# Kernel tuning notes

Measured on AMD Instinct MI355X. Metric: run time of the kernel, lower is better.

Reference implementation:

```python
import jax, jax.numpy as jnp
import numpy as np

N_NODES = 50000
N_EDGES = 600000
N_FEAT = 256
N_HID = 128
N_CLASS = 64
HEADS = 8
LEAKY_SLOPE = 0.2


def setup_inputs() -> dict:
    key = jax.random.key(0)
    ks = jax.random.split(key, 12)
    D0 = N_HID // HEADS  # 16 per-head dim, layer 0
    x = jax.random.normal(ks[0], (N_NODES, N_FEAT), dtype=jnp.float32)
    edge_index = jax.random.randint(ks[1], (2, N_EDGES), 0, N_NODES, dtype=jnp.int64)
    s0 = 1.0 / np.sqrt(N_FEAT)
    s1 = 1.0 / np.sqrt(N_HID)
    return {
        "x": x,
        "edge_index": edge_index,
        "W0": jax.random.normal(ks[2], (N_FEAT, HEADS * D0), dtype=jnp.float32) * s0,
        "a_src0": jax.random.normal(ks[3], (HEADS, D0), dtype=jnp.float32) * s0,
        "a_dst0": jax.random.normal(ks[4], (HEADS, D0), dtype=jnp.float32) * s0,
        "b0": jnp.zeros((HEADS * D0,), dtype=jnp.float32),
        "W1": jax.random.normal(ks[5], (N_HID, HEADS * N_CLASS), dtype=jnp.float32) * s1,
        "a_src1": jax.random.normal(ks[6], (HEADS, N_CLASS), dtype=jnp.float32) * s1,
        "a_dst1": jax.random.normal(ks[7], (HEADS, N_CLASS), dtype=jnp.float32) * s1,
        "b1": jnp.zeros((N_CLASS,), dtype=jnp.float32),
    }


def gat_conv(x, src, dst, W, a_s, a_d, b, concat, num_nodes):
    H, D = a_s.shape
    h = (x @ W).reshape(-1, H, D)                    # [N, H, D]
    alpha_s = jnp.einsum('nhd,hd->nh', h, a_s)       # [N, H]
    alpha_d = jnp.einsum('nhd,hd->nh', h, a_d)       # [N, H]
    e = jax.nn.leaky_relu(alpha_s[src] + alpha_d[dst], LEAKY_SLOPE)  # [E, H]
    # numerically stable edge-softmax grouped by destination node
    m = jax.ops.segment_max(e, dst, num_segments=num_nodes)
    m = jnp.where(jnp.isfinite(m), m, 0.0)           # nodes with no in-edges
    ex = jnp.exp(e - m[dst])
    denom = jax.ops.segment_sum(ex, dst, num_segments=num_nodes)
    alpha = ex / (denom[dst] + 1e-16)                # [E, H]
    msg = h[src] * alpha[:, :, None]                 # [E, H, D]
    out = jax.ops.segment_sum(msg, dst, num_segments=num_nodes)  # [N, H, D]
    if concat:
        out = out.reshape(num_nodes, H * D)
    else:
        out = out.mean(axis=1)
    return out + b


def reference(x, edge_index, W0, a_src0, a_dst0, b0, W1, a_src1, a_dst1, b1):
    src, dst = edge_index[0], edge_index[1]
    h = gat_conv(x, src, dst, W0, a_src0, a_dst0, b0, True, N_NODES)
    h = jax.nn.elu(h)  # eval mode: dropout is identity
    h = gat_conv(h, src, dst, W1, a_src1, a_dst1, b1, False, N_NODES)
    return jax.nn.log_softmax(h, axis=-1)
```

## Files before the change

kernel.cpp:

```cpp
#include <hip/hip_runtime.h>
#include <hip/hip_bf16.h>
#include <math.h>

#define NN 50000
#define NE 600000
#define NF 256
#define NHID 128
#define HEADS 8
#define D0 16
#define NCLS 64
#define NB1 196

#define PK0 (9 * 8 * 64 * 8)
#define PK1 (4 * 32 * 64 * 8)
#define PKA (4 * 64 * 8)
#define CASTN (NN * NF / 4)
#define PREPN (PK0 + PK1 + PKA)

typedef __attribute__((ext_vector_type(8))) short short8;
typedef __attribute__((ext_vector_type(4))) float floatx4;

__device__ __forceinline__ float bf16lo(uint v) { return __uint_as_float((v & 0xffffu) << 16); }
__device__ __forceinline__ float bf16hi(uint v) { return __uint_as_float(v & 0xffff0000u); }
__device__ __forceinline__ uint packbf16(float a, float b) {
    return (uint)__bfloat16_as_ushort(__float2bfloat16(a)) |
           ((uint)__bfloat16_as_ushort(__float2bfloat16(b)) << 16);
}
__device__ __forceinline__ short f2bf(float v) {
    return (short)__bfloat16_as_ushort(__float2bfloat16(v));
}
__device__ __forceinline__ float bf16tof(short v) {
    return __uint_as_float(((uint)(ushort)v) << 16);
}


__global__ void scan1_kernel(const int* __restrict__ deg, int* __restrict__ rs,
                             int* __restrict__ bsum) {
    __shared__ int sh[256];
    int tid = threadIdx.x;
    int i = blockIdx.x * 256 + tid;
    int v = (i < NN) ? deg[i] : 0;
    sh[tid] = v;
    __syncthreads();
    for (int off = 1; off < 256; off <<= 1) {
        int t = (tid >= off) ? sh[tid - off] : 0;
        __syncthreads();
        sh[tid] += t;
        __syncthreads();
    }
    if (i < NN) rs[i] = sh[tid] - v;
    if (tid == 255) bsum[blockIdx.x] = sh[255];
}

__global__ void scan2_kernel(const int* __restrict__ bsum, int* __restrict__ bsumx) {
    __shared__ int sh[256];
    int tid = threadIdx.x;
    int v = (tid < NB1) ? bsum[tid] : 0;
    sh[tid] = v;
    __syncthreads();
    for (int off = 1; off < 256; off <<= 1) {
        int t = (tid >= off) ? sh[tid - off] : 0;
        __syncthreads();
        sh[tid] += t;
        __syncthreads();
    }
    if (tid < NB1) bsumx[tid] = sh[tid] - v;
}

__global__ void scan3_kernel(int* __restrict__ rs, const int* __restrict__ bsumx) {
    int i = blockIdx.x * 256 + threadIdx.x;
    if (i < NN) rs[i] += bsumx[i >> 8];
}

__global__ void scatter_kernel(const int* __restrict__ ei, const int* __restrict__ rs,
                               int* __restrict__ cnt2, int* __restrict__ csr) {
    int e = blockIdx.x * 256 + threadIdx.x;
    if (e >= NE) return;
    int s = ei[e], d = ei[NE + e];
    int pos = rs[d] + atomicAdd(&cnt2[d], 1);
    csr[pos] = s;
}


__global__ void fused_prep_kernel(const float* __restrict__ x, short* __restrict__ xb,
                                  const int* __restrict__ ei, int* __restrict__ deg,
                                  const float* __restrict__ W0, const float* __restrict__ aS0,
                                  const float* __restrict__ aD0, const float* __restrict__ W1,
                                  const float* __restrict__ aS1, const float* __restrict__ aD1,
                                  short* __restrict__ Bp0, short* __restrict__ Bp1,
                                  short* __restrict__ wA1b) {
    int i = blockIdx.x * 256 + threadIdx.x;
    if (i < CASTN) {
        float4 v = ((const float4*)x)[i];
        short4 r;
        r.x = f2bf(v.x); r.y = f2bf(v.y); r.z = f2bf(v.z); r.w = f2bf(v.w);
        ((short4*)xb)[i] = r;
        return;
    }
    int e = i - CASTN;
    if (e < NE) {
        atomicAdd(&deg[ei[NE + e]], 1);
        return;
    }
    int tid = e - NE;
    if (tid < PK0) {
        int j = tid & 7, l = (tid >> 3) & 63, ks = (tid >> 9) & 7, t = tid >> 12;
        int k = ks * 32 + (l >> 4) * 8 + j;
        float v;
        if (t < 8) {
            int c = t * 16 + (l & 15);
            v = W0[(size_t)k * 128 + c];
        } else {
            int jj = l & 15;
            int hh = jj & 7;
            const float* av = (jj < 8) ? aS0 : aD0;
            float sum = 0.f;
            for (int dd = 0; dd < D0; ++dd)
                sum += W0[(size_t)k * 128 + hh * D0 + dd] * av[hh * D0 + dd];
            v = sum;
        }
        Bp0[tid] = f2bf(v);
    } else if (tid < PK0 + PK1) {
        int t2 = tid - PK0;
        int j = t2 & 7, l = (t2 >> 3) & 63, ks = (t2 >> 9) & 31, t = t2 >> 14;
        int kk = ks * 32 + (l >> 4) * 8 + j;
        int c = t * 16 + (l & 15);
        Bp1[t2] = f2bf(W1[(size_t)(kk & 127) * 512 + (kk >> 7) * 64 + c] * 0.125f);
    } else if (tid < PREPN) {
        int t3 = tid - PK0 - PK1;
        int j = t3 & 7, l = (t3 >> 3) & 63, ks = t3 >> 9;
        int k = ks * 32 + (l >> 4) * 8 + j;
        int c = l & 15;
        int h = c & 7;
        const float* av = (c < 8) ? aS1 : aD1;
        float sum = 0.f;
        for (int d2 = 0; d2 < NCLS; ++d2)
            sum += W1[(size_t)k * 512 + h * NCLS + d2] * av[h * NCLS + d2];
        wA1b[t3] = f2bf(sum);
    }
}


__global__ __launch_bounds__(256) void gemm0_mfma(const short* __restrict__ xb,
                                                  const short* __restrict__ Bp,
                                                  ushort* __restrict__ h0b,
                                                  float* __restrict__ as0,
                                                  float* __restrict__ ad0) {
    int lane = threadIdx.x & 63, wave = threadIdx.x >> 6;
    int rg = wave >> 1, cg = wave & 1;
    int q = lane >> 4, c16 = lane & 15;
    int row0 = blockIdx.x * 32 + rg * 16;
    int arow = row0 + c16;
    if (arow > NN - 1) arow = NN - 1;
    const short* ap = xb + (size_t)arow * NF + q * 8;
    floatx4 acc[5] = {};
#pragma unroll
    for (int ks = 0; ks < 8; ++ks) {
        short8 af = *(const short8*)(ap + ks * 32);
#pragma unroll
        for (int tt = 0; tt < 4; ++tt) {
            int t = cg * 4 + tt;
            short8 bf = *(const short8*)(Bp + (((size_t)t * 8 + ks) * 64 + lane) * 8);
            acc[tt] = __builtin_amdgcn_mfma_f32_16x16x32_bf16(af, bf, acc[tt], 0, 0, 0);
        }
        if (cg) {
            short8 bf = *(const short8*)(Bp + (((size_t)8 * 8 + ks) * 64 + lane) * 8);
            acc[4] = __builtin_amdgcn_mfma_f32_16x16x32_bf16(af, bf, acc[4], 0, 0, 0);
        }
    }
#pragma unroll
    for (int r = 0; r < 4; ++r) {
        int grow = row0 + q * 4 + r;
        if (grow >= NN) continue;
#pragma unroll
        for (int tt = 0; tt < 4; ++tt)
            h0b[(size_t)grow * NHID + cg * 64 + tt * 16 + c16] =
                (ushort)f2bf(acc[tt][r]);
        if (cg) {
            float v = acc[4][r];
            if (c16 < 8) as0[grow * 8 + c16] = v;
            else         ad0[grow * 8 + (c16 - 8)] = v;
        }
    }
}

__global__ __launch_bounds__(256) void alpha1_mfma(const ushort* __restrict__ x1b,
                                                   const short* __restrict__ wA1b,
                                                   float* __restrict__ as1,
                                                   float* __restrict__ ad1) {
    int lane = threadIdx.x & 63, wave = threadIdx.x >> 6;
    int q = lane >> 4, c16 = lane & 15;
    int row0 = blockIdx.x * 64 + wave * 16;
    int arow = row0 + c16;
    if (arow > NN - 1) arow = NN - 1;
    const short* ap = (const short*)x1b + (size_t)arow * NHID + q * 8;
    floatx4 acc = {};
#pragma unroll
    for (int ks = 0; ks < 4; ++ks) {
        short8 af = *(const short8*)(ap + ks * 32);
        short8 bf = *(const short8*)(wA1b + (((size_t)ks) * 64 + lane) * 8);
        acc = __builtin_amdgcn_mfma_f32_16x16x32_bf16(af, bf, acc, 0, 0, 0);
    }
#pragma unroll
    for (int r = 0; r < 4; ++r) {
        int grow = row0 + q * 4 + r;
        if (grow >= NN) continue;
        float v = acc[r];
        if (c16 < 8) as1[grow * 8 + c16] = v;
        else         ad1[grow * 8 + (c16 - 8)] = v;
    }
}

__global__ __launch_bounds__(256) void gemm1_mfma(const short* __restrict__ AGG,
                                                  const short* __restrict__ Bp,
                                                  const float* __restrict__ b1,
                                                  float* __restrict__ out) {
    int lane = threadIdx.x & 63, wave = threadIdx.x >> 6;
    int q = lane >> 4, c16 = lane & 15;
    int row0 = blockIdx.x * 64 + wave * 16;
    int arow = row0 + c16;
    if (arow > NN - 1) arow = NN - 1;
    const short* ap = AGG + (size_t)arow * 1024 + q * 8;
    floatx4 acc[4] = {};
    for (int ks = 0; ks < 32; ++ks) {
        short8 af = *(const short8*)(ap + ks * 32);
#pragma unroll
        for (int t = 0; t < 4; ++t) {
            short8 bf = *(const short8*)(Bp + (((size_t)t * 32 + ks) * 64 + lane) * 8);
            acc[t] = __builtin_amdgcn_mfma_f32_16x16x32_bf16(af, bf, acc[t], 0, 0, 0);
        }
    }
    float bias[4];
#pragma unroll
    for (int t = 0; t < 4; ++t) bias[t] = b1[t * 16 + c16];
#pragma unroll
    for (int r = 0; r < 4; ++r) {
        int grow = row0 + q * 4 + r;
        float z[4];
        float mx = -INFINITY;
#pragma unroll
        for (int t = 0; t < 4; ++t) {
            z[t] = acc[t][r] + bias[t];
            mx = fmaxf(mx, z[t]);
        }
        mx = fmaxf(mx, __shfl_xor(mx, 1));
        mx = fmaxf(mx, __shfl_xor(mx, 2));
        mx = fmaxf(mx, __shfl_xor(mx, 4));
        mx = fmaxf(mx, __shfl_xor(mx, 8));
        float s = 0.f;
#pragma unroll
        for (int t = 0; t < 4; ++t) s += expf(z[t] - mx);
        s += __shfl_xor(s, 1);
        s += __shfl_xor(s, 2);
        s += __shfl_xor(s, 4);
        s += __shfl_xor(s, 8);
        float lse = mx + logf(s);
        if (grow < NN) {
#pragma unroll
            for (int t = 0; t < 4; ++t)
                out[(size_t)grow * NCLS + t * 16 + c16] = z[t] - lse;
        }
    }
}


__global__ __launch_bounds__(256) void fused_edge0(
    const int* __restrict__ rs, const int* __restrict__ deg, const int* __restrict__ csr,
    const ushort* __restrict__ h0b, const float* __restrict__ as0, const float* __restrict__ ad0,
    const float* __restrict__ b0, ushort* __restrict__ x1b) {
    int d = (blockIdx.x * 256 + threadIdx.x) >> 6;
    int lane = threadIdx.x & 63;
    if (d >= NN) return;
    int row = rs[d], dg = deg[d];
    int hl = lane & 7, g = lane >> 3;
    int hp = lane >> 3;
    float adv = ad0[d * 8 + hl];
    float den = 0.f;
    float2 acc = {0.f, 0.f};
    for (int base = 0; base < dg; base += 8) {
        int i = base + g;
        int s = (i < dg) ? csr[row + i] : 0;
        float ev = as0[s * 8 + hl] + adv;
        ev = ev > 0.f ? ev : 0.2f * ev;
        float p = (i < dg) ? __expf(ev) : 0.f;
        den += p;
        uint vbuf[8];
#pragma unroll
        for (int g2 = 0; g2 < 8; ++g2) {
            int sg = __builtin_amdgcn_readlane(s, g2 * 8);
            vbuf[g2] = *(const uint*)(h0b + (size_t)sg * NHID + 2 * lane);
        }
#pragma unroll
        for (int g2 = 0; g2 < 8; ++g2) {
            float ph = __shfl(p, g2 * 8 + hp);
            acc.x += bf16lo(vbuf[g2]) * ph;
            acc.y += bf16hi(vbuf[g2]) * ph;
        }
    }
    den += __shfl_xor(den, 8);
    den += __shfl_xor(den, 16);
    den += __shfl_xor(den, 32);
    float dh = __shfl(den, hp);
    float inv = 1.f / (dh + 1e-16f);
    float2 bb = ((const float2*)b0)[lane];
    float o0 = acc.x * inv + bb.x;
    float o1 = acc.y * inv + bb.y;
    o0 = o0 > 0.f ? o0 : expf(o0) - 1.f;
    o1 = o1 > 0.f ? o1 : expf(o1) - 1.f;
    *(uint*)(x1b + (size_t)d * NHID + 2 * lane) = packbf16(o0, o1);
}

__global__ __launch_bounds__(256) void fused_edge1(
    const int* __restrict__ rs, const int* __restrict__ deg, const int* __restrict__ csr,
    const ushort* __restrict__ x1b, const float* __restrict__ as1, const float* __restrict__ ad1,
    ushort* __restrict__ AGG) {
    int gw = (blockIdx.x * 256 + threadIdx.x) >> 6;
    int lane = threadIdx.x & 63;
    int dA = 2 * gw;
    if (dA >= NN) return;
    int dB = dA + 1;
    int q = lane >> 4, c16 = lane & 15, h7 = lane & 7;
    int d_l = (lane >= 32) ? dB : dA;
    int row_l = rs[d_l], dg_l = deg[d_l];
    bool V = ((lane & 8) == 0) == (lane < 32);
    float adv = ad1[d_l * 8 + h7];
    int dgA = __shfl(dg_l, 0);
    int dgB = __shfl(dg_l, 32);
    int dgmax = dgA > dgB ? dgA : dgB;
    float den = 0.f;
    floatx4 acc[8] = {};
    for (int base = 0; base < dgmax; base += 16) {
        short8 af;
        int sarr[8];
#pragma unroll
        for (int j = 0; j < 8; ++j) {
            int idx = base + (q & 1) * 8 + j;
            int s = 0;
            if (idx < dg_l) s = csr[row_l + idx];
            sarr[j] = s;
            float ev = as1[s * 8 + h7] + adv;
            ev = ev > 0.f ? ev : 0.2f * ev;
            float p = __expf(ev);
            p = (idx < dg_l && V) ? p : 0.f;
            short pb = f2bf(p);
            af[j] = pb;
            den += bf16tof(pb);
        }
#pragma unroll
        for (int t = 0; t < 8; ++t) {
            short8 bv;
#pragma unroll
            for (int j = 0; j < 8; ++j)
                bv[j] = (short)x1b[(size_t)sarr[j] * NHID + t * 16 + c16];
            acc[t] = __builtin_amdgcn_mfma_f32_16x16x32_bf16(af, bv, acc[t], 0, 0, 0);
        }
    }
    den += __shfl_xor(den, 8);
    den += __shfl_xor(den, 16);
    int hbase = (q & 1) * 4;
#pragma unroll
    for (int r = 0; r < 4; ++r) {
        int hh = hbase + r;
        float dh = __shfl(den, (lane & 32) + hh);
        float inv = 1.f / (dh + 1e-16f);
        size_t base_a = (size_t)d_l * 1024 + (size_t)hh * 128 + c16;
#pragma unroll
        for (int t = 0; t < 8; ++t)
            AGG[base_a + t * 16] = (ushort)f2bf(acc[t][r] * inv);
    }
}


extern "C" void kernel_launch(void* const* d_in, const int* in_sizes, int n_in,
                              void* d_out, int out_size, void* d_ws, size_t ws_size,
                              hipStream_t stream) {
    const float* x   = (const float*)d_in[0];
    const int*   ei  = (const int*)d_in[1];
    const float* W0  = (const float*)d_in[2];
    const float* aS0 = (const float*)d_in[3];
    const float* aD0 = (const float*)d_in[4];
    const float* b0  = (const float*)d_in[5];
    const float* W1  = (const float*)d_in[6];
    const float* aS1 = (const float*)d_in[7];
    const float* aD1 = (const float*)d_in[8];
    const float* b1  = (const float*)d_in[9];
    float* out = (float*)d_out;

    char* ws = (char*)d_ws;
    ushort* x1b = (ushort*)ws; ws += (size_t)NN * NHID * 2;
    ushort* h0b = (ushort*)ws; ws += (size_t)NN * NHID * 2;
    ushort* AGG = (ushort*)ws; ws += (size_t)NN * 1024 * 2;
    short* xb   = (short*)ws; ws += (size_t)NN * NF * 2;
    float* as0  = (float*)ws; ws += (size_t)NN * HEADS * 4;
    float* ad0  = (float*)ws; ws += (size_t)NN * HEADS * 4;
    float* as1  = (float*)ws; ws += (size_t)NN * HEADS * 4;
    float* ad1  = (float*)ws; ws += (size_t)NN * HEADS * 4;
    short* Bp0  = (short*)ws; ws += (size_t)PK0 * 2;
    short* Bp1  = (short*)ws; ws += (size_t)PK1 * 2;
    short* wA1b = (short*)ws; ws += (size_t)PKA * 2;
    int* deg    = (int*)ws; ws += (size_t)NN * 4;
    int* cnt2   = (int*)ws; ws += (size_t)NN * 4;
    int* rs     = (int*)ws; ws += (size_t)NN * 4;
    int* bsum   = (int*)ws; ws += 256 * 4;
    int* bsumx  = (int*)ws; ws += 256 * 4;
    int* csr    = (int*)ws; ws += (size_t)NE * 4;

    const int FUSEDN = CASTN + NE + PREPN;

    hipMemsetAsync(deg, 0, (size_t)2 * NN * 4, stream);
    fused_prep_kernel<<<(FUSEDN + 255) / 256, 256, 0, stream>>>(
        x, xb, ei, deg, W0, aS0, aD0, W1, aS1, aD1, Bp0, Bp1, wA1b);

    scan1_kernel<<<NB1, 256, 0, stream>>>(deg, rs, bsum);
    scan2_kernel<<<1, 256, 0, stream>>>(bsum, bsumx);
    scan3_kernel<<<NB1, 256, 0, stream>>>(rs, bsumx);
    scatter_kernel<<<(NE + 255) / 256, 256, 0, stream>>>(ei, rs, cnt2, csr);

    gemm0_mfma<<<(NN + 31) / 32, 256, 0, stream>>>(xb, Bp0, h0b, as0, ad0);
    fused_edge0<<<(NN + 3) / 4, 256, 0, stream>>>(rs, deg, csr, h0b, as0, ad0, b0, x1b);

    alpha1_mfma<<<(NN + 63) / 64, 256, 0, stream>>>(x1b, wA1b, as1, ad1);
    fused_edge1<<<(NN / 2 + 3) / 4, 256, 0, stream>>>(rs, deg, csr, x1b, as1, ad1, AGG);
    gemm1_mfma<<<(NN + 63) / 64, 256, 0, stream>>>((const short*)AGG, Bp1, b1, out);
}
```

Measured before the change: 325.6 us.

## Fuse layer-1 projection GEMM and log-softmax into edge aggregation kernel

The per-node aggregated head features (1024 bf16 per node) now go into LDS instead of a global AGG buffer, and each wave runs the W1 projection MFMA and log-softmax on its two nodes. This removes the large AGG write/read round trip and one kernel launch. In exchange, each wave does a 16-row MFMA where only 2 rows are useful (heavy MFMA waste), reloads the whole Bp1 per wave pair of nodes, and adds LDS pressure.

```diff
diff --git a/kernel.cpp b/kernel.cpp
--- a/kernel.cpp
+++ b/kernel.cpp
@@ -208,58 +208,6 @@
         float v = acc[r];
         if (c16 < 8) as1[grow * 8 + c16] = v;
         else         ad1[grow * 8 + (c16 - 8)] = v;
-    }
-}
-
-__global__ __launch_bounds__(256) void gemm1_mfma(const short* __restrict__ AGG,
-                                                  const short* __restrict__ Bp,
-                                                  const float* __restrict__ b1,
-                                                  float* __restrict__ out) {
-    int lane = threadIdx.x & 63, wave = threadIdx.x >> 6;
-    int q = lane >> 4, c16 = lane & 15;
-    int row0 = blockIdx.x * 64 + wave * 16;
-    int arow = row0 + c16;
-    if (arow > NN - 1) arow = NN - 1;
-    const short* ap = AGG + (size_t)arow * 1024 + q * 8;
-    floatx4 acc[4] = {};
-    for (int ks = 0; ks < 32; ++ks) {
-        short8 af = *(const short8*)(ap + ks * 32);
-#pragma unroll
-        for (int t = 0; t < 4; ++t) {
-            short8 bf = *(const short8*)(Bp + (((size_t)t * 32 + ks) * 64 + lane) * 8);
-            acc[t] = __builtin_amdgcn_mfma_f32_16x16x32_bf16(af, bf, acc[t], 0, 0, 0);
-        }
-    }
-    float bias[4];
-#pragma unroll
-    for (int t = 0; t < 4; ++t) bias[t] = b1[t * 16 + c16];
-#pragma unroll
-    for (int r = 0; r < 4; ++r) {
-        int grow = row0 + q * 4 + r;
-        float z[4];
-        float mx = -INFINITY;
-#pragma unroll
-        for (int t = 0; t < 4; ++t) {
-            z[t] = acc[t][r] + bias[t];
-            mx = fmaxf(mx, z[t]);
-        }
-        mx = fmaxf(mx, __shfl_xor(mx, 1));
-        mx = fmaxf(mx, __shfl_xor(mx, 2));
-        mx = fmaxf(mx, __shfl_xor(mx, 4));
-        mx = fmaxf(mx, __shfl_xor(mx, 8));
-        float s = 0.f;
-#pragma unroll
-        for (int t = 0; t < 4; ++t) s += expf(z[t] - mx);
-        s += __shfl_xor(s, 1);
-        s += __shfl_xor(s, 2);
-        s += __shfl_xor(s, 4);
-        s += __shfl_xor(s, 8);
-        float lse = mx + logf(s);
-        if (grow < NN) {
-#pragma unroll
-            for (int t = 0; t < 4; ++t)
-                out[(size_t)grow * NCLS + t * 16 + c16] = z[t] - lse;
-        }
     }
 }
 
@@ -313,8 +261,10 @@
 __global__ __launch_bounds__(256) void fused_edge1(
     const int* __restrict__ rs, const int* __restrict__ deg, const int* __restrict__ csr,
     const ushort* __restrict__ x1b, const float* __restrict__ as1, const float* __restrict__ ad1,
-    ushort* __restrict__ AGG) {
+    const short* __restrict__ Bp1, const float* __restrict__ b1, float* __restrict__ out) {
+    __shared__ ushort aggNsh[4][2][1024];
     int gw = (blockIdx.x * 256 + threadIdx.x) >> 6;
+    int wave = threadIdx.x >> 6;
     int lane = threadIdx.x & 63;
     int dA = 2 * gw;
     if (dA >= NN) return;
@@ -358,15 +308,58 @@
     den += __shfl_xor(den, 8);
     den += __shfl_xor(den, 16);
     int hbase = (q & 1) * 4;
+    int drow = lane >> 5;
 #pragma unroll
     for (int r = 0; r < 4; ++r) {
         int hh = hbase + r;
         float dh = __shfl(den, (lane & 32) + hh);
         float inv = 1.f / (dh + 1e-16f);
-        size_t base_a = (size_t)d_l * 1024 + (size_t)hh * 128 + c16;
 #pragma unroll
         for (int t = 0; t < 8; ++t)
-            AGG[base_a + t * 16] = (ushort)f2bf(acc[t][r] * inv);
+            aggNsh[wave][drow][hh * 128 + t * 16 + c16] = (ushort)f2bf(acc[t][r] * inv);
+    }
+    asm volatile("" ::: "memory");
+    int rsel = c16 & 1;
+    const short* abase = (const short*)&aggNsh[wave][rsel][q * 8];
+    floatx4 acc2[4] = {};
+    for (int ks = 0; ks < 32; ++ks) {
+        short8 af2 = *(const short8*)(abase + ks * 32);
+#pragma unroll
+        for (int t = 0; t < 4; ++t) {
+            short8 bf = *(const short8*)(Bp1 + (((size_t)t * 32 + ks) * 64 + lane) * 8);
+            acc2[t] = __builtin_amdgcn_mfma_f32_16x16x32_bf16(af2, bf, acc2[t], 0, 0, 0);
+        }
+    }
+    float bias2[4];
+#pragma unroll
+    for (int t = 0; t < 4; ++t) bias2[t] = b1[t * 16 + c16];
+#pragma unroll
+    for (int r2 = 0; r2 < 2; ++r2) {
+        int dd = (r2 == 0) ? dA : dB;
+        float z[4];
+        float mx = -INFINITY;
+#pragma unroll
+        for (int t = 0; t < 4; ++t) {
+            z[t] = acc2[t][r2] + bias2[t];
+            mx = fmaxf(mx, z[t]);
+        }
+        mx = fmaxf(mx, __shfl_xor(mx, 1));
+        mx = fmaxf(mx, __shfl_xor(mx, 2));
+        mx = fmaxf(mx, __shfl_xor(mx, 4));
+        mx = fmaxf(mx, __shfl_xor(mx, 8));
+        float s = 0.f;
+#pragma unroll
+        for (int t = 0; t < 4; ++t) s += expf(z[t] - mx);
+        s += __shfl_xor(s, 1);
+        s += __shfl_xor(s, 2);
+        s += __shfl_xor(s, 4);
+        s += __shfl_xor(s, 8);
+        float lse = mx + logf(s);
+        if (q == 0) {
+#pragma unroll
+            for (int t = 0; t < 4; ++t)
+                out[(size_t)dd * NCLS + t * 16 + c16] = z[t] - lse;
+        }
     }
 }
 
@@ -389,7 +382,6 @@
     char* ws = (char*)d_ws;
     ushort* x1b = (ushort*)ws; ws += (size_t)NN * NHID * 2;
     ushort* h0b = (ushort*)ws; ws += (size_t)NN * NHID * 2;
-    ushort* AGG = (ushort*)ws; ws += (size_t)NN * 1024 * 2;
     short* xb   = (short*)ws; ws += (size_t)NN * NF * 2;
     float* as0  = (float*)ws; ws += (size_t)NN * HEADS * 4;
     float* ad0  = (float*)ws; ws += (size_t)NN * HEADS * 4;
@@ -420,6 +412,6 @@
     fused_edge0<<<(NN + 3) / 4, 256, 0, stream>>>(rs, deg, csr, h0b, as0, ad0, b0, x1b);
 
     alpha1_mfma<<<(NN + 63) / 64, 256, 0, stream>>>(x1b, wA1b, as1, ad1);
-    fused_edge1<<<(NN / 2 + 3) / 4, 256, 0, stream>>>(rs, deg, csr, x1b, as1, ad1, AGG);
-    gemm1_mfma<<<(NN + 63) / 64, 256, 0, stream>>>((const short*)AGG, Bp1, b1, out);
-}
+    fused_edge1<<<(NN / 2 + 3) / 4, 256, 0, stream>>>(rs, deg, csr, x1b, as1, ad1,
+                                                      Bp1, b1, out);
+}
```

Measured after the change: 366.6 us. 1.13x slower.
